# Kernel tuning notes

Hardware: AMD Instinct MI355X
Metric: run time of the kernel (lower is better)

Reference implementation:

```python
import jax, jax.numpy as jnp
import numpy as np

B, D, H, W, C = 2, 16, 16, 16, 64
CBAR = 32


def setup_inputs() -> dict:
    key = jax.random.key(0)
    ks = jax.random.split(key, 6)
    x = jax.random.normal(ks[0], (B, D, H, W, C), dtype=jnp.float32)
    # 1x1x1 Conv3D == per-voxel linear over channels; scale for stable softmax
    Wf = jax.random.normal(ks[1], (C, CBAR), dtype=jnp.float32) / np.sqrt(C)
    Wg = jax.random.normal(ks[2], (C, CBAR), dtype=jnp.float32) / np.sqrt(C)
    Wh = jax.random.normal(ks[3], (C, CBAR), dtype=jnp.float32) / np.sqrt(C)
    Wo = jax.random.normal(ks[4], (CBAR, C), dtype=jnp.float32) / np.sqrt(CBAR)
    bf = jnp.zeros((CBAR,), jnp.float32)
    bg = jnp.zeros((CBAR,), jnp.float32)
    bh = jnp.zeros((CBAR,), jnp.float32)
    bo = jnp.zeros((C,), jnp.float32)
    gamma = jnp.ones((), jnp.float32)
    return {"x": x, "Wf": Wf, "bf": bf, "Wg": Wg, "bg": bg,
            "Wh": Wh, "bh": bh, "Wo": Wo, "bo": bo, "gamma": gamma}


def reference(x, Wf, bf, Wg, bg, Wh, bh, Wo, bo, gamma):
    b, d, h, w, c = x.shape
    n = d * h * w
    xf = x.reshape(b, n, c)                       # [B, N, C]
    f = xf @ Wf + bf                              # [B, N, cbar] (keys)
    g = xf @ Wg + bg                              # [B, N, cbar] (queries)
    hv = xf @ Wh + bh                             # [B, N, cbar] (values)
    s = jnp.einsum('bqc,bkc->bqk', g, f)          # [B, N, N]
    beta = jax.nn.softmax(s, axis=-1)
    bhv = jnp.einsum('bqk,bkc->bqc', beta, hv)    # [B, N, cbar]
    o = bhv @ Wo + bo                             # [B, N, C]
    out = xf + gamma * o
    return out.reshape(b, d, h, w, c)
```

## Files before the change

### kernel.cpp

```cpp
#include <hip/hip_runtime.h>
#include <hip/hip_bf16.h>

typedef short short8 __attribute__((ext_vector_type(8)));
typedef float f32x4 __attribute__((ext_vector_type(4)));

__device__ __forceinline__ float bf2f(unsigned short v) {
    unsigned int u = ((unsigned int)v) << 16;
    float f;
    __builtin_memcpy(&f, &u, 4);
    return f;
}

__device__ __forceinline__ unsigned short f2bf(float f) {
    unsigned int u;
    __builtin_memcpy(&u, &f, 4);
    u += 0x7fffu + ((u >> 16) & 1u);
    return (unsigned short)(u >> 16);
}

__device__ __forceinline__ unsigned int pack2(float a, float b) {
    return (unsigned int)f2bf(a) | ((unsigned int)f2bf(b) << 16);
}

__device__ __forceinline__ unsigned int pack_trunc(float a, float b) {
    unsigned int ua, ub;
    __builtin_memcpy(&ua, &a, 4);
    __builtin_memcpy(&ub, &b, 4);
    return __builtin_amdgcn_perm(ub, ua, 0x07060302u);
}

__device__ __forceinline__ void split2(float a, float b,
                                       unsigned int& hi, unsigned int& lo) {
    unsigned short ah = f2bf(a), bh = f2bf(b);
    float al = a - bf2f(ah), bl = b - bf2f(bh);
    hi = (unsigned int)ah | ((unsigned int)bh << 16);
    lo = (unsigned int)f2bf(al) | ((unsigned int)f2bf(bl) << 16);
}

__device__ __forceinline__ float loadv(const void* p, int idx, bool is_fp32) {
    return is_fp32 ? ((const float*)p)[idx] : bf2f(((const unsigned short*)p)[idx]);
}
__device__ __forceinline__ bool detect_fp32(const void* x, int tid, int* flag_sh) {
    if (tid < 64) {
        unsigned int w = ((const unsigned int*)x)[tid];
        unsigned int e = (w >> 7) & 0xFFu;
        unsigned long long m = __ballot(e > 140u);
        if (tid == 0) *flag_sh = (__popcll(m) >= 8) ? 1 : 0;
    }
    __syncthreads();
    return *flag_sh != 0;
}

__global__ __launch_bounds__(128) void proj_kernel(
    const void* __restrict__ x,
    const void* __restrict__ Wf, const void* __restrict__ bfv,
    const void* __restrict__ Wg, const void* __restrict__ bgv,
    const void* __restrict__ Wh, const void* __restrict__ bhv,
    unsigned short* __restrict__ F, unsigned short* __restrict__ G,
    unsigned short* __restrict__ Ht) {
    __shared__ unsigned int WTh[3 * 32 * 36];
    __shared__ unsigned int WTl[3 * 32 * 36];
    __shared__ float bL[96];
    __shared__ int dflag;
    int tid = threadIdx.x;
    bool fp32 = detect_fp32(x, tid, &dflag);
    int lane = tid & 63, wave = tid >> 6;
    int Q = lane >> 4, l15 = lane & 15;
    int row0 = (blockIdx.x * 2 + wave) << 4;

    const void* Ws[3] = {Wf, Wg, Wh};
    const void* bs[3] = {bfv, bgv, bhv};

    for (int i = tid; i < 3072; i += 128) {
        int m = i >> 10;
        int r = i & 1023;
        int p = r >> 5, n = r & 31;
        float e0 = loadv(Ws[m], (2 * p) * 32 + n, fp32);
        float e1 = loadv(Ws[m], (2 * p + 1) * 32 + n, fp32);
        unsigned int hi, lo;
        split2(e0, e1, hi, lo);
        WTh[(m * 32 + n) * 36 + p] = hi;
        WTl[(m * 32 + n) * 36 + p] = lo;
    }
    if (tid < 96) bL[tid] = loadv(bs[tid >> 5], tid & 31, fp32);

    short8 a0h, a0l, a1h, a1l;
    {
        int base = (row0 + l15) * 64 + Q * 8;
        union { unsigned int u[4]; short8 s8; } A0h, A0l, A1h, A1l;
        if (fp32) {
            const float* xf = (const float*)x;
            f32x4 v0 = *(const f32x4*)(xf + base);
            f32x4 v1 = *(const f32x4*)(xf + base + 4);
            f32x4 w0 = *(const f32x4*)(xf + base + 32);
            f32x4 w1 = *(const f32x4*)(xf + base + 36);
            split2(v0[0], v0[1], A0h.u[0], A0l.u[0]);
            split2(v0[2], v0[3], A0h.u[1], A0l.u[1]);
            split2(v1[0], v1[1], A0h.u[2], A0l.u[2]);
            split2(v1[2], v1[3], A0h.u[3], A0l.u[3]);
            split2(w0[0], w0[1], A1h.u[0], A1l.u[0]);
            split2(w0[2], w0[3], A1h.u[1], A1l.u[1]);
            split2(w1[0], w1[1], A1h.u[2], A1l.u[2]);
            split2(w1[2], w1[3], A1h.u[3], A1l.u[3]);
        } else {
            const unsigned short* xb = (const unsigned short*)x;
            A0h.s8 = *(const short8*)(xb + base);
            A1h.s8 = *(const short8*)(xb + base + 32);
            A0l.u[0] = A0l.u[1] = A0l.u[2] = A0l.u[3] = 0;
            A1l = A0l;
        }
        a0h = A0h.s8; a0l = A0l.s8; a1h = A1h.s8; a1l = A1l.s8;
    }
    __syncthreads();

#pragma unroll
    for (int m = 0; m < 3; m++) {
#pragma unroll
        for (int cb = 0; cb < 2; cb++) {
            int rowbase = (m * 32 + cb * 16 + l15) * 36;
            union { uint4 v; short8 s8; } B0h, B0l, B1h, B1l;
            B0h.v = *(const uint4*)&WTh[rowbase + Q * 4];
            B1h.v = *(const uint4*)&WTh[rowbase + 16 + Q * 4];
            B0l.v = *(const uint4*)&WTl[rowbase + Q * 4];
            B1l.v = *(const uint4*)&WTl[rowbase + 16 + Q * 4];
            f32x4 z = {0.f, 0.f, 0.f, 0.f};
            f32x4 acc = __builtin_amdgcn_mfma_f32_16x16x32_bf16(a0h, B0h.s8, z, 0, 0, 0);
            acc = __builtin_amdgcn_mfma_f32_16x16x32_bf16(a0h, B0l.s8, acc, 0, 0, 0);
            acc = __builtin_amdgcn_mfma_f32_16x16x32_bf16(a0l, B0h.s8, acc, 0, 0, 0);
            acc = __builtin_amdgcn_mfma_f32_16x16x32_bf16(a1h, B1h.s8, acc, 0, 0, 0);
            acc = __builtin_amdgcn_mfma_f32_16x16x32_bf16(a1h, B1l.s8, acc, 0, 0, 0);
            acc = __builtin_amdgcn_mfma_f32_16x16x32_bf16(a1l, B1h.s8, acc, 0, 0, 0);
            float bias = bL[m * 32 + cb * 16 + l15];
            if (m < 2) {
                unsigned short* dst = (m == 0) ? F : G;
#pragma unroll
                for (int r = 0; r < 4; r++)
                    dst[(row0 + Q * 4 + r) * 32 + cb * 16 + l15] = f2bf(acc[r] + bias);
            } else {
                int b = row0 >> 12;
                int n0 = (row0 & 4095) + Q * 4;
                uint2 pk;
                pk.x = pack2(acc[0] + bias, acc[1] + bias);
                pk.y = pack2(acc[2] + bias, acc[3] + bias);
                *(uint2*)(Ht + b * 131072 + (cb * 16 + l15) * 4096 + n0) = pk;
            }
        }
    }
}

__global__ __launch_bounds__(512, 2) void attn_kernel(
    const unsigned short* __restrict__ F, const unsigned short* __restrict__ G,
    const unsigned short* __restrict__ Ht,
    const void* __restrict__ x,
    const void* __restrict__ Wo, const void* __restrict__ bo,
    const void* __restrict__ gamma_p,
    void* __restrict__ out) {
    __shared__ __attribute__((aligned(16))) unsigned short P_sh[8][2][16][40];
    __shared__ float O_lds[8][32][32];
    __shared__ float l_lds[8][32];
    __shared__ float Om[32][33];
    __shared__ float lmg[32];
    __shared__ float WoL[32][64];
    __shared__ float boL[64];
    __shared__ int dflag;

    int tid = threadIdx.x;
    bool fp32 = detect_fp32(x, tid, &dflag);

    for (int i = tid; i < 2048; i += 512) WoL[i >> 6][i & 63] = loadv(Wo, i, fp32);
    if (tid < 64) boL[tid] = loadv(bo, tid, fp32);

    int bx = blockIdx.x;
    int b = bx >> 7;
    int q0 = (bx & 127) << 5;
    int wave = tid >> 6;
    int lane = tid & 63;
    int Q = lane >> 4, l15 = lane & 15;

    const unsigned short* Fb = F + (b << 17);
    const unsigned short* Gb = G + (b << 17);
    const unsigned short* Htb = Ht + (b << 17);

    short8 g0 = *(const short8*)(Gb + ((q0 + l15) << 5) + (Q << 3));
    short8 g1 = *(const short8*)(Gb + ((q0 + 16 + l15) << 5) + (Q << 3));

    f32x4 O00 = {0.f, 0.f, 0.f, 0.f}, O01 = O00, O10 = O00, O11 = O00;
    float ls0 = 0.f, ls1 = 0.f;

    int k_begin = wave << 9;
    short8 af0 = *(const short8*)(Fb + ((k_begin + l15) << 5) + (Q << 3));
    short8 af1 = *(const short8*)(Fb + ((k_begin + 16 + l15) << 5) + (Q << 3));
    short8 bh0 = *(const short8*)(Htb + (l15 << 12) + k_begin + (Q << 3));
    short8 bh1 = *(const short8*)(Htb + ((16 + l15) << 12) + k_begin + (Q << 3));

    for (int it = 0; it < 16; ++it) {
        int itn = (it < 15) ? it + 1 : 15;
        int kn = k_begin + (itn << 5);
        short8 naf0 = *(const short8*)(Fb + ((kn + l15) << 5) + (Q << 3));
        short8 naf1 = *(const short8*)(Fb + ((kn + 16 + l15) << 5) + (Q << 3));
        short8 nbh0 = *(const short8*)(Htb + (l15 << 12) + kn + (Q << 3));
        short8 nbh1 = *(const short8*)(Htb + ((16 + l15) << 12) + kn + (Q << 3));

        f32x4 z = {0.f, 0.f, 0.f, 0.f};
        f32x4 c00 = __builtin_amdgcn_mfma_f32_16x16x32_bf16(af0, g0, z, 0, 0, 0);
        f32x4 c01 = __builtin_amdgcn_mfma_f32_16x16x32_bf16(af1, g0, z, 0, 0, 0);
        f32x4 c10 = __builtin_amdgcn_mfma_f32_16x16x32_bf16(af0, g1, z, 0, 0, 0);
        f32x4 c11 = __builtin_amdgcn_mfma_f32_16x16x32_bf16(af1, g1, z, 0, 0, 0);

        float e00[4], e01[4], e10[4], e11[4];
#pragma unroll
        for (int r = 0; r < 4; r++) {
            e00[r] = __expf(c00[r]); e01[r] = __expf(c01[r]);
            e10[r] = __expf(c10[r]); e11[r] = __expf(c11[r]);
            ls0 += e00[r] + e01[r];
            ls1 += e10[r] + e11[r];
        }

        uint2 w0, w1;
        w0.x = pack_trunc(e00[0], e00[1]); w0.y = pack_trunc(e00[2], e00[3]);
        w1.x = pack_trunc(e01[0], e01[1]); w1.y = pack_trunc(e01[2], e01[3]);
        *(uint2*)&P_sh[wave][0][l15][Q * 4] = w0;
        *(uint2*)&P_sh[wave][0][l15][16 + Q * 4] = w1;
        uint2 w2, w3;
        w2.x = pack_trunc(e10[0], e10[1]); w2.y = pack_trunc(e10[2], e10[3]);
        w3.x = pack_trunc(e11[0], e11[1]); w3.y = pack_trunc(e11[2], e11[3]);
        *(uint2*)&P_sh[wave][1][l15][Q * 4] = w2;
        *(uint2*)&P_sh[wave][1][l15][16 + Q * 4] = w3;

        short8 pf0 = *(const short8*)&P_sh[wave][0][l15][Q * 8];
        short8 pf1 = *(const short8*)&P_sh[wave][1][l15][Q * 8];

        O00 = __builtin_amdgcn_mfma_f32_16x16x32_bf16(pf0, bh0, O00, 0, 0, 0);
        O01 = __builtin_amdgcn_mfma_f32_16x16x32_bf16(pf0, bh1, O01, 0, 0, 0);
        O10 = __builtin_amdgcn_mfma_f32_16x16x32_bf16(pf1, bh0, O10, 0, 0, 0);
        O11 = __builtin_amdgcn_mfma_f32_16x16x32_bf16(pf1, bh1, O11, 0, 0, 0);

        af0 = naf0; af1 = naf1; bh0 = nbh0; bh1 = nbh1;
    }

    ls0 += __shfl_xor(ls0, 16); ls0 += __shfl_xor(ls0, 32);
    ls1 += __shfl_xor(ls1, 16); ls1 += __shfl_xor(ls1, 32);
    if (Q == 0) {
        l_lds[wave][l15] = ls0;
        l_lds[wave][16 + l15] = ls1;
    }
#pragma unroll
    for (int r = 0; r < 4; r++) {
        O_lds[wave][(Q << 2) | r][l15]             = O00[r];
        O_lds[wave][(Q << 2) | r][16 + l15]        = O01[r];
        O_lds[wave][16 + ((Q << 2) | r)][l15]      = O10[r];
        O_lds[wave][16 + ((Q << 2) | r)][16 + l15] = O11[r];
    }
    __syncthreads();

    if (tid < 32) {
        float s = 0.f;
#pragma unroll
        for (int w = 0; w < 8; w++) s += l_lds[w][tid];
        lmg[tid] = 1.0f / s;
    }
#pragma unroll
    for (int idx = tid; idx < 1024; idx += 512) {
        int q = idx >> 5, c = idx & 31;
        float s = 0.f;
#pragma unroll
        for (int w = 0; w < 8; w++) s += O_lds[w][q][c];
        Om[q][c] = s;
    }
    __syncthreads();

    int q = tid >> 4;
    int ch = (tid & 15) << 2;
    float a0 = 0.f, a1 = 0.f, a2 = 0.f, a3 = 0.f;
#pragma unroll
    for (int c = 0; c < 32; c++) {
        float ob = Om[q][c];
        f32x4 wr = *(const f32x4*)&WoL[c][ch];
        a0 += ob * wr[0]; a1 += ob * wr[1]; a2 += ob * wr[2]; a3 += ob * wr[3];
    }
    float inv = lmg[q];
    float gam = loadv(gamma_p, 0, fp32);
    int gq = q0 + q;
    int obase = (((b << 12) + gq) << 6) + ch;
    if (fp32) {
        f32x4 xv = *(const f32x4*)((const float*)x + obase);
        f32x4 ov;
        ov[0] = xv[0] + gam * (a0 * inv + boL[ch + 0]);
        ov[1] = xv[1] + gam * (a1 * inv + boL[ch + 1]);
        ov[2] = xv[2] + gam * (a2 * inv + boL[ch + 2]);
        ov[3] = xv[3] + gam * (a3 * inv + boL[ch + 3]);
        *(f32x4*)((float*)out + obase) = ov;
    } else {
        const unsigned short* xb = (const unsigned short*)x;
        unsigned short* ob16 = (unsigned short*)out;
        uint2 pk;
        pk.x = pack2(bf2f(xb[obase + 0]) + gam * (a0 * inv + boL[ch + 0]),
                     bf2f(xb[obase + 1]) + gam * (a1 * inv + boL[ch + 1]));
        pk.y = pack2(bf2f(xb[obase + 2]) + gam * (a2 * inv + boL[ch + 2]),
                     bf2f(xb[obase + 3]) + gam * (a3 * inv + boL[ch + 3]));
        *(uint2*)(ob16 + obase) = pk;
    }
}

extern "C" void kernel_launch(void* const* d_in, const int* in_sizes, int n_in,
                              void* d_out, int out_size, void* d_ws, size_t ws_size,
                              hipStream_t stream) {
    const void* x   = d_in[0];
    const void* Wf  = d_in[1];
    const void* bfv = d_in[2];
    const void* Wg  = d_in[3];
    const void* bgv = d_in[4];
    const void* Wh  = d_in[5];
    const void* bhv = d_in[6];
    const void* Wo  = d_in[7];
    const void* bo  = d_in[8];
    const void* gam = d_in[9];

    unsigned short* F  = (unsigned short*)d_ws;
    unsigned short* G  = F + 262144;
    unsigned short* Ht = G + 262144;

    proj_kernel<<<256, 128, 0, stream>>>(x, Wf, bfv, Wg, bgv, Wh, bhv, F, G, Ht);
    attn_kernel<<<256, 512, 0, stream>>>(F, G, Ht, x, Wo, bo, gam, d_out);
}
```

Before: 99.79 us.

## Fuse projection and attention kernels into one cooperative launch with grid sync

Merges the projection kernel and the attention kernel into a single cooperative kernel. Each 512-thread block computes the F/G/Ht projections for 32 rows, spread across its 8 waves, then waits at a grid-wide barrier before running the attention phase. This removes one kernel launch and the inter-kernel gap. In exchange it adds the cost of a grid sync, a larger LDS footprint per block, and a cooperative launch that requires all 256 blocks to be co-resident.

```diff
diff --git a/kernel.cpp b/kernel.cpp
--- a/kernel.cpp
+++ b/kernel.cpp
@@ -1,5 +1,8 @@
 #include <hip/hip_runtime.h>
 #include <hip/hip_bf16.h>
+#include <hip/hip_cooperative_groups.h>
+
+namespace cg = cooperative_groups;
 
 typedef short short8 __attribute__((ext_vector_type(8)));
 typedef float f32x4 __attribute__((ext_vector_type(4)));
@@ -51,27 +54,36 @@
     return *flag_sh != 0;
 }
 
-__global__ __launch_bounds__(128) void proj_kernel(
+__global__ __launch_bounds__(512, 2) void fused_kernel(
     const void* __restrict__ x,
     const void* __restrict__ Wf, const void* __restrict__ bfv,
     const void* __restrict__ Wg, const void* __restrict__ bgv,
     const void* __restrict__ Wh, const void* __restrict__ bhv,
+    const void* __restrict__ Wo, const void* __restrict__ bo,
+    const void* __restrict__ gamma_p,
     unsigned short* __restrict__ F, unsigned short* __restrict__ G,
-    unsigned short* __restrict__ Ht) {
+    unsigned short* __restrict__ Ht, void* __restrict__ out) {
     __shared__ unsigned int WTh[3 * 32 * 36];
     __shared__ unsigned int WTl[3 * 32 * 36];
     __shared__ float bL[96];
     __shared__ int dflag;
+    __shared__ __attribute__((aligned(16))) unsigned short P_sh[8][2][16][40];
+    __shared__ float O_lds[8][32][32];
+    __shared__ float l_lds[8][32];
+    __shared__ float Om[32][33];
+    __shared__ float lmg[32];
+    __shared__ float WoL[32][64];
+    __shared__ float boL[64];
+
     int tid = threadIdx.x;
     bool fp32 = detect_fp32(x, tid, &dflag);
     int lane = tid & 63, wave = tid >> 6;
     int Q = lane >> 4, l15 = lane & 15;
-    int row0 = (blockIdx.x * 2 + wave) << 4;
 
     const void* Ws[3] = {Wf, Wg, Wh};
     const void* bs[3] = {bfv, bgv, bhv};
 
-    for (int i = tid; i < 3072; i += 128) {
+    for (int i = tid; i < 3072; i += 512) {
         int m = i >> 10;
         int r = i & 1023;
         int p = r >> 5, n = r & 31;
@@ -82,8 +94,12 @@
         WTh[(m * 32 + n) * 36 + p] = hi;
         WTl[(m * 32 + n) * 36 + p] = lo;
     }
+    for (int i = tid; i < 2048; i += 512) WoL[i >> 6][i & 63] = loadv(Wo, i, fp32);
     if (tid < 96) bL[tid] = loadv(bs[tid >> 5], tid & 31, fp32);
-
+    if (tid < 64) boL[tid] = loadv(bo, tid, fp32);
+
+    int rt = wave >> 2;
+    int row0 = (blockIdx.x << 5) + (rt << 4);
     short8 a0h, a0l, a1h, a1l;
     {
         int base = (row0 + l15) * 64 + Q * 8;
@@ -113,69 +129,44 @@
     }
     __syncthreads();
 
-#pragma unroll
-    for (int m = 0; m < 3; m++) {
-#pragma unroll
-        for (int cb = 0; cb < 2; cb++) {
-            int rowbase = (m * 32 + cb * 16 + l15) * 36;
-            union { uint4 v; short8 s8; } B0h, B0l, B1h, B1l;
-            B0h.v = *(const uint4*)&WTh[rowbase + Q * 4];
-            B1h.v = *(const uint4*)&WTh[rowbase + 16 + Q * 4];
-            B0l.v = *(const uint4*)&WTl[rowbase + Q * 4];
-            B1l.v = *(const uint4*)&WTl[rowbase + 16 + Q * 4];
-            f32x4 z = {0.f, 0.f, 0.f, 0.f};
-            f32x4 acc = __builtin_amdgcn_mfma_f32_16x16x32_bf16(a0h, B0h.s8, z, 0, 0, 0);
-            acc = __builtin_amdgcn_mfma_f32_16x16x32_bf16(a0h, B0l.s8, acc, 0, 0, 0);
-            acc = __builtin_amdgcn_mfma_f32_16x16x32_bf16(a0l, B0h.s8, acc, 0, 0, 0);
-            acc = __builtin_amdgcn_mfma_f32_16x16x32_bf16(a1h, B1h.s8, acc, 0, 0, 0);
-            acc = __builtin_amdgcn_mfma_f32_16x16x32_bf16(a1h, B1l.s8, acc, 0, 0, 0);
-            acc = __builtin_amdgcn_mfma_f32_16x16x32_bf16(a1l, B1h.s8, acc, 0, 0, 0);
-            float bias = bL[m * 32 + cb * 16 + l15];
-            if (m < 2) {
-                unsigned short* dst = (m == 0) ? F : G;
-#pragma unroll
-                for (int r = 0; r < 4; r++)
-                    dst[(row0 + Q * 4 + r) * 32 + cb * 16 + l15] = f2bf(acc[r] + bias);
-            } else {
-                int b = row0 >> 12;
-                int n0 = (row0 & 4095) + Q * 4;
-                uint2 pk;
-                pk.x = pack2(acc[0] + bias, acc[1] + bias);
-                pk.y = pack2(acc[2] + bias, acc[3] + bias);
-                *(uint2*)(Ht + b * 131072 + (cb * 16 + l15) * 4096 + n0) = pk;
-            }
+    auto proj_tile = [&](int m, int cb) {
+        int rowbase = (m * 32 + cb * 16 + l15) * 36;
+        union { uint4 v; short8 s8; } B0h, B0l, B1h, B1l;
+        B0h.v = *(const uint4*)&WTh[rowbase + Q * 4];
+        B1h.v = *(const uint4*)&WTh[rowbase + 16 + Q * 4];
+        B0l.v = *(const uint4*)&WTl[rowbase + Q * 4];
+        B1l.v = *(const uint4*)&WTl[rowbase + 16 + Q * 4];
+        f32x4 z = {0.f, 0.f, 0.f, 0.f};
+        f32x4 acc = __builtin_amdgcn_mfma_f32_16x16x32_bf16(a0h, B0h.s8, z, 0, 0, 0);
+        acc = __builtin_amdgcn_mfma_f32_16x16x32_bf16(a0h, B0l.s8, acc, 0, 0, 0);
+        acc = __builtin_amdgcn_mfma_f32_16x16x32_bf16(a0l, B0h.s8, acc, 0, 0, 0);
+        acc = __builtin_amdgcn_mfma_f32_16x16x32_bf16(a1h, B1h.s8, acc, 0, 0, 0);
+        acc = __builtin_amdgcn_mfma_f32_16x16x32_bf16(a1h, B1l.s8, acc, 0, 0, 0);
+        acc = __builtin_amdgcn_mfma_f32_16x16x32_bf16(a1l, B1h.s8, acc, 0, 0, 0);
+        float bias = bL[m * 32 + cb * 16 + l15];
+        if (m < 2) {
+            unsigned short* dst = (m == 0) ? F : G;
+#pragma unroll
+            for (int r = 0; r < 4; r++)
+                dst[(row0 + Q * 4 + r) * 32 + cb * 16 + l15] = f2bf(acc[r] + bias);
+        } else {
+            int bb = row0 >> 12;
+            int n0 = (row0 & 4095) + Q * 4;
+            uint2 pk;
+            pk.x = pack2(acc[0] + bias, acc[1] + bias);
+            pk.y = pack2(acc[2] + bias, acc[3] + bias);
+            *(uint2*)(Ht + bb * 131072 + (cb * 16 + l15) * 4096 + n0) = pk;
         }
-    }
-}
-
-__global__ __launch_bounds__(512, 2) void attn_kernel(
-    const unsigned short* __restrict__ F, const unsigned short* __restrict__ G,
-    const unsigned short* __restrict__ Ht,
-    const void* __restrict__ x,
-    const void* __restrict__ Wo, const void* __restrict__ bo,
-    const void* __restrict__ gamma_p,
-    void* __restrict__ out) {
-    __shared__ __attribute__((aligned(16))) unsigned short P_sh[8][2][16][40];
-    __shared__ float O_lds[8][32][32];
-    __shared__ float l_lds[8][32];
-    __shared__ float Om[32][33];
-    __shared__ float lmg[32];
-    __shared__ float WoL[32][64];
-    __shared__ float boL[64];
-    __shared__ int dflag;
-
-    int tid = threadIdx.x;
-    bool fp32 = detect_fp32(x, tid, &dflag);
-
-    for (int i = tid; i < 2048; i += 512) WoL[i >> 6][i & 63] = loadv(Wo, i, fp32);
-    if (tid < 64) boL[tid] = loadv(bo, tid, fp32);
+    };
+    int c4 = wave & 3;
+    proj_tile(c4 >> 1, c4 & 1);
+    if (c4 < 2) proj_tile(2, c4);
+
+    cg::this_grid().sync();
 
     int bx = blockIdx.x;
     int b = bx >> 7;
     int q0 = (bx & 127) << 5;
-    int wave = tid >> 6;
-    int lane = tid & 63;
-    int Q = lane >> 4, l15 = lane & 15;
 
     const unsigned short* Fb = F + (b << 17);
     const unsigned short* Gb = G + (b << 17);
@@ -319,7 +310,10 @@
     unsigned short* F  = (unsigned short*)d_ws;
     unsigned short* G  = F + 262144;
     unsigned short* Ht = G + 262144;
-
-    proj_kernel<<<256, 128, 0, stream>>>(x, Wf, bfv, Wg, bgv, Wh, bhv, F, G, Ht);
-    attn_kernel<<<256, 512, 0, stream>>>(F, G, Ht, x, Wo, bo, gam, d_out);
-}
+    void* outp = d_out;
+
+    void* args[14] = {&x, &Wf, &bfv, &Wg, &bgv, &Wh, &bhv, &Wo, &bo, &gam,
+                      &F, &G, &Ht, &outp};
+    hipLaunchCooperativeKernel((const void*)fused_kernel, dim3(256), dim3(512),
+                               args, 0u, stream);
+}
```

After: 139.4 us. 1.4x slower.
